# Performance work log

Measured on AMD Instinct MI355X. Metric: run time of the kernel, lower is better.

The kernel has to match this reference:

```python
import jax, jax.numpy as jnp
import numpy as np

ALPHA = 3.0
NNODES, DIM, K = 8192, 64, 32


def setup_inputs() -> dict:
    key = jax.random.key(0)
    ks = jax.random.split(key, 8)
    return {
        "idx": jnp.arange(NNODES, dtype=jnp.int64) if jax.config.jax_enable_x64 else jnp.arange(NNODES, dtype=jnp.int32),
        "emb1": jax.random.normal(ks[0], (NNODES, DIM), dtype=jnp.float32),
        "emb2": jax.random.normal(ks[1], (NNODES, DIM), dtype=jnp.float32),
        "lin1_w": jax.random.normal(ks[2], (DIM, DIM), dtype=jnp.float32) * 0.1,
        "lin1_b": jax.random.normal(ks[3], (DIM,), dtype=jnp.float32) * 0.1,
        "lin2_w": jax.random.normal(ks[4], (DIM, DIM), dtype=jnp.float32) * 0.1,
        "lin2_b": jax.random.normal(ks[5], (DIM,), dtype=jnp.float32) * 0.1,
        "noise": jax.random.uniform(ks[6], (NNODES, NNODES), dtype=jnp.float32),
        "k": K,
    }


def reference(idx, emb1, emb2, lin1_w, lin1_b, lin2_w, lin2_b, noise, k):
    # gather node embeddings, project, tanh(alpha * .)
    nodevec1 = jnp.tanh(ALPHA * (emb1[idx] @ lin1_w.T + lin1_b))  # [N, D]
    nodevec2 = jnp.tanh(ALPHA * (emb2[idx] @ lin2_w.T + lin2_b))  # [N, D]
    # antisymmetric bilinear score
    a = nodevec1 @ nodevec2.T - nodevec2 @ nodevec1.T             # [N, N]
    adj = jax.nn.relu(jnp.tanh(ALPHA * a))                         # [N, N]
    n = adj.shape[0]
    # topk per row with uniform tie-break noise (torch: adj + rand*0.01)
    _, t1 = jax.lax.top_k(adj + noise * 0.01, k)                   # [N, k] int
    rows = jnp.arange(n)[:, None]                                  # [N, 1]
    mask = jnp.zeros((n, n), dtype=adj.dtype).at[rows, t1].set(1.0)
    adj = adj * mask + jnp.eye(n, dtype=adj.dtype)
    return adj
```

## Files before the change

kernel.cpp:

```cpp
#include <hip/hip_runtime.h>

#define NN 8192
#define DD 64
#define CC 128
#define XCLAMP 7.99881172180175781f

__device__ __forceinline__ float guard(float v) {
    asm volatile("" : "+v"(v));
    return v;
}

__device__ __forceinline__ float xla_tanhf(float x) {
    float xc = fminf(fmaxf(x, -XCLAMP), XCLAMP);
    float x2 = xc * xc;
    float p = fmaf(x2, -2.76076847742355e-16f, 2.00018790482477e-13f);
    p = fmaf(x2, p, -8.60467152213735e-11f);
    p = fmaf(x2, p, 5.12229709037114e-08f);
    p = fmaf(x2, p, 1.48572235717979e-05f);
    p = fmaf(x2, p, 6.37261928875436e-04f);
    p = fmaf(x2, p, 4.89352455891786e-03f);
    p = xc * p;
    float q = fmaf(x2, 1.19825839466702e-06f, 1.18534705686654e-04f);
    q = fmaf(x2, q, 2.26843463243900e-03f);
    q = fmaf(x2, q, 4.89352518554385e-03f);
    float r = p / q;
    return (fabsf(x) < 0.0004f) ? x : r;
}

__device__ __forceinline__ float score_of(float a, float nz) {
    float adj = fmaxf(xla_tanhf(3.0f * a), 0.0f);
    float m = guard(0.01f * nz);
    return adj + m;
}

__global__ __launch_bounds__(256) void k1_nodevec(
    const int* __restrict__ idx,
    const float* __restrict__ emb1, const float* __restrict__ emb2,
    const float* __restrict__ w1, const float* __restrict__ b1,
    const float* __restrict__ w2, const float* __restrict__ b2,
    float* __restrict__ Wt)
{
    __shared__ float sw1[64 * 65], sw2[64 * 65];
    __shared__ float sb1[64], sb2[64];
    __shared__ float se1[4][64], se2[4][64];
    int t = threadIdx.x;
    for (int i = t; i < 4096; i += 256) {
        int r = i >> 6, c = i & 63;
        sw1[r * 65 + c] = w1[i];
        sw2[r * 65 + c] = w2[i];
    }
    if (t < 64) { sb1[t] = b1[t]; sb2[t] = b2[t]; }
    int nl = t >> 6, d = t & 63;
    int n = blockIdx.x * 4 + nl;
    bool is64 = (idx[1] == 0);
    int g = (is64 ? idx[2 * n] : idx[n]) & 8191;
    se1[nl][d] = emb1[g * 64 + d];
    se2[nl][d] = emb2[g * 64 + d];
    __syncthreads();
    float z1 = 0.0f, z2 = 0.0f;
#pragma unroll 16
    for (int q = 0; q < 64; ++q) {
        z1 = fmaf(se1[nl][q], sw1[d * 65 + q], z1);
        z2 = fmaf(se2[nl][q], sw2[d * 65 + q], z2);
    }
    z1 = 3.0f * guard(z1 + sb1[d]);
    z2 = 3.0f * guard(z2 + sb2[d]);
    Wt[(size_t)d * NN + n]        = xla_tanhf(z1);
    Wt[(size_t)(64 + d) * NN + n] = xla_tanhf(z2);
}

__global__ __launch_bounds__(256) void k_init(
    float* __restrict__ listVal, int* __restrict__ listIdx)
{
    int i = blockIdx.x * 256 + threadIdx.x;
    listVal[i] = -1.0f;
    listIdx[i] = -1;
}

__global__ __launch_bounds__(512) void k2p_pairscore(
    const float* __restrict__ Wt, const float* __restrict__ noise,
    float* __restrict__ Sc)
{
    __shared__ __align__(16) float smem[17024];
    float* sA1 = smem;
    float* sB1 = smem + 4224;
    float* sA2 = smem + 8448;
    float* sB2 = smem + 12672;
    int bx = blockIdx.x, by = blockIdx.y;
    if (bx < by) return;
    int R = by * 128, C = bx * 128;
    int t = threadIdx.x;
    int ty = t >> 5, tx = t & 31;

    float A1[8][4], A2[8][4];
#pragma unroll
    for (int i = 0; i < 8; ++i)
#pragma unroll
        for (int j = 0; j < 4; ++j) { A1[i][j] = 0.0f; A2[i][j] = 0.0f; }

    for (int kc = 0; kc < 2; ++kc) {
        int k0 = kc * 32;
#pragma unroll
        for (int p = 0; p < 2; ++p) {
            int q = p * 512 + t;
            int kf = q >> 5;
            int rr = (q & 31) * 4;
            float4 v1 = *(const float4*)&Wt[(size_t)(k0 + kf) * NN + R + rr];
            *(float4*)&sA1[kf * 132 + rr] = v1;
            float4 v2 = *(const float4*)&Wt[(size_t)(64 + k0 + kf) * NN + C + rr];
            *(float4*)&sB1[kf * 132 + rr] = v2;
            float4 v3 = *(const float4*)&Wt[(size_t)(64 + k0 + kf) * NN + R + rr];
            *(float4*)&sA2[kf * 132 + rr] = v3;
            float4 v4 = *(const float4*)&Wt[(size_t)(k0 + kf) * NN + C + rr];
            *(float4*)&sB2[kf * 132 + rr] = v4;
        }
        __syncthreads();
#pragma unroll 4
        for (int kk = 0; kk < 32; ++kk) {
            float4 a10 = *(const float4*)&sA1[kk * 132 + ty * 8];
            float4 a11 = *(const float4*)&sA1[kk * 132 + ty * 8 + 4];
            float4 b1v = *(const float4*)&sB1[kk * 132 + tx * 4];
            float4 a20 = *(const float4*)&sA2[kk * 132 + ty * 8];
            float4 a21 = *(const float4*)&sA2[kk * 132 + ty * 8 + 4];
            float4 b2v = *(const float4*)&sB2[kk * 132 + tx * 4];
            float a1[8] = {a10.x, a10.y, a10.z, a10.w, a11.x, a11.y, a11.z, a11.w};
            float b1[4] = {b1v.x, b1v.y, b1v.z, b1v.w};
            float a2[8] = {a20.x, a20.y, a20.z, a20.w, a21.x, a21.y, a21.z, a21.w};
            float b2[4] = {b2v.x, b2v.y, b2v.z, b2v.w};
#pragma unroll
            for (int i = 0; i < 8; ++i)
#pragma unroll
                for (int j = 0; j < 4; ++j) {
                    A1[i][j] = fmaf(a1[i], b1[j], A1[i][j]);
                    A2[i][j] = fmaf(a2[i], b2[j], A2[i][j]);
                }
        }
        __syncthreads();
    }

    float* dT = smem;
#pragma unroll
    for (int i = 0; i < 8; ++i) {
        int I = ty * 8 + i;
        int grow = R + I;
        float4 nz = *(const float4*)&noise[(size_t)grow * NN + C + tx * 4];
        float4 o;
#pragma unroll
        for (int j = 0; j < 4; ++j) {
            float d  = guard(A1[i][j] - A2[i][j]);
            float ta = xla_tanhf(3.0f * fabsf(d));
            float adj1 = (d > 0.0f) ? ta : 0.0f;
            float adj2 = (d < 0.0f) ? ta : 0.0f;
            float m = guard(0.01f * ((const float*)&nz)[j]);
            ((float*)&o)[j] = adj1 + m;
            dT[(tx * 4 + j) * 133 + I] = adj2;
        }
        *(float4*)&Sc[(size_t)grow * NN + C + tx * 4] = o;
    }
    __syncthreads();

    int c4 = tx * 4;
#pragma unroll
    for (int rr = 0; rr < 8; ++rr) {
        int r2 = rr * 16 + ty;
        int grow = C + r2;
        float4 nz = *(const float4*)&noise[(size_t)grow * NN + R + c4];
        float4 o;
        o.x = dT[r2 * 133 + c4 + 0] + guard(0.01f * nz.x);
        o.y = dT[r2 * 133 + c4 + 1] + guard(0.01f * nz.y);
        o.z = dT[r2 * 133 + c4 + 2] + guard(0.01f * nz.z);
        o.w = dT[r2 * 133 + c4 + 3] + guard(0.01f * nz.w);
        *(float4*)&Sc[(size_t)grow * NN + R + c4] = o;
    }
}

__global__ __launch_bounds__(256) void k3_screen(
    const float* __restrict__ Sc,
    float* __restrict__ listVal, int* __restrict__ listIdx)
{
    int lane = threadIdx.x & 63;
    int w    = threadIdx.x >> 6;
    int row  = blockIdx.x * 4 + w;
    const float* Srow = Sc + (size_t)row * NN;

    float Lv = listVal[row * 64 + lane];
    int   Lj = listIdx[row * 64 + lane];

    for (int c0 = 0; c0 < NN; c0 += 256) {
        float s0 = Srow[c0 + lane];
        float s1 = Srow[c0 + 64 + lane];
        float s2 = Srow[c0 + 128 + lane];
        float s3 = Srow[c0 + 192 + lane];
#pragma unroll
        for (int u = 0; u < 4; ++u) {
            float s = (u == 0) ? s0 : (u == 1) ? s1 : (u == 2) ? s2 : s3;
            int jb = c0 + u * 64;
            float tau = __shfl(Lv, 63);
            unsigned long long m = __ballot(s > tau);
            while (m) {
                int b = __ffsll((unsigned long long)m) - 1;
                m &= m - 1;
                float v = __shfl(s, b);
                tau = __shfl(Lv, 63);
                if (v > tau) {
                    float Lu = __shfl_up(Lv, 1);
                    int   Ju = __shfl_up(Lj, 1);
                    bool ge  = (Lv >= v);
                    bool geu = (lane == 0) || (Lu >= v);
                    float nv = ge ? Lv : (geu ? v : Lu);
                    int   nj = ge ? Lj : (geu ? (jb + b) : Ju);
                    Lv = nv; Lj = nj;
                }
            }
        }
    }
    listVal[row * 64 + lane] = Lv;
    listIdx[row * 64 + lane] = Lj;
}

__global__ __launch_bounds__(256) void k4a_fill(float* __restrict__ out)
{
    int i4 = blockIdx.x * 256 + threadIdx.x;
    int f0 = i4 * 4;
    int row = f0 >> 13;
    int colbase = f0 & 8191;
    int drel = row - colbase;
    float4 z = make_float4(0.f, 0.f, 0.f, 0.f);
    if (drel >= 0 && drel < 4) ((float*)&z)[drel] = 1.0f;
    *(float4*)&out[f0] = z;
}

__global__ __launch_bounds__(256) void k4b_scatter(
    const int* __restrict__ listIdx, const float* __restrict__ listVal,
    const float* __restrict__ noise, const int* __restrict__ kptr,
    float* __restrict__ out)
{
    int lane = threadIdx.x & 63;
    int w    = threadIdx.x >> 6;
    int row  = blockIdx.x * 4 + w;
    int kk = kptr[0]; if (kk > 64) kk = 64; if (kk < 1) kk = 1;
    if (lane < kk) {
        int   j = listIdx[row * 64 + lane] & 8191;
        float s = listVal[row * 64 + lane];
        float nz = noise[(size_t)row * NN + j];
        float m = guard(0.01f * nz);
        float adj = s - m;
        if (j == row) adj += 1.0f;
        out[(size_t)row * NN + j] = adj;
    }
}

extern "C" void kernel_launch(void* const* d_in, const int* in_sizes, int n_in,
                              void* d_out, int out_size, void* d_ws, size_t ws_size,
                              hipStream_t stream) {
    (void)in_sizes; (void)n_in; (void)out_size; (void)ws_size;
    const int*   idx   = (const int*)d_in[0];
    const float* emb1  = (const float*)d_in[1];
    const float* emb2  = (const float*)d_in[2];
    const float* w1    = (const float*)d_in[3];
    const float* b1    = (const float*)d_in[4];
    const float* w2    = (const float*)d_in[5];
    const float* b2    = (const float*)d_in[6];
    const float* noise = (const float*)d_in[7];
    const int*   kptr  = (const int*)d_in[8];

    float* out = (float*)d_out;
    float* Sc  = out;

    char*  ws      = (char*)d_ws;
    float* Wt      = (float*)ws;
    float* listVal = (float*)(ws + (size_t)4 * 1024 * 1024);
    int*   listIdx = (int*)  (ws + (size_t)6 * 1024 * 1024);

    k1_nodevec<<<NN / 4, 256, 0, stream>>>(idx, emb1, emb2, w1, b1, w2, b2, Wt);
    k_init<<<NN * 64 / 256, 256, 0, stream>>>(listVal, listIdx);

    dim3 gp(64, 64);
    k2p_pairscore<<<gp, 512, 0, stream>>>(Wt, noise, Sc);

    k3_screen<<<NN / 4, 256, 0, stream>>>(Sc, listVal, listIdx);

    k4a_fill<<<65536, 256, 0, stream>>>(out);
    k4b_scatter<<<NN / 4, 256, 0, stream>>>(listIdx, listVal, noise, kptr, out);
}
```

Baseline: 485.4 us.

## Restructure pair-score GEMM to 256 threads with 8x8 register tiles

The antisymmetric pair-score kernel now uses 256 threads, each computing an 8x8 tile for both products instead of 8x4. It streams a single A/B shared-memory buffer over four K-chunks, using padded B rows to reduce bank conflicts. The transposed lower-triangle output is staged through shared memory in four slices to keep LDS use small. This raises per-thread arithmetic intensity and cuts LDS traffic per FMA, at the cost of higher register pressure (128 accumulators), possibly lower occupancy, and extra barriers.

```diff
diff --git a/kernel.cpp b/kernel.cpp
--- a/kernel.cpp
+++ b/kernel.cpp
@@ -27,12 +27,6 @@
     return (fabsf(x) < 0.0004f) ? x : r;
 }
 
-__device__ __forceinline__ float score_of(float a, float nz) {
-    float adj = fmaxf(xla_tanhf(3.0f * a), 0.0f);
-    float m = guard(0.01f * nz);
-    return adj + m;
-}
-
 __global__ __launch_bounds__(256) void k1_nodevec(
     const int* __restrict__ idx,
     const float* __restrict__ emb1, const float* __restrict__ emb2,
@@ -77,100 +71,116 @@
     listIdx[i] = -1;
 }
 
-__global__ __launch_bounds__(512) void k2p_pairscore(
+__global__ __launch_bounds__(256) void k2p_pairscore(
     const float* __restrict__ Wt, const float* __restrict__ noise,
     float* __restrict__ Sc)
 {
-    __shared__ __align__(16) float smem[17024];
-    float* sA1 = smem;
-    float* sB1 = smem + 4224;
-    float* sA2 = smem + 8448;
-    float* sB2 = smem + 12672;
+    __shared__ __align__(16) float smem[32 * 128 + 32 * 144];
+    float* sA = smem;
+    float* sB = smem + 32 * 128;
     int bx = blockIdx.x, by = blockIdx.y;
     if (bx < by) return;
     int R = by * 128, C = bx * 128;
     int t = threadIdx.x;
-    int ty = t >> 5, tx = t & 31;
-
-    float A1[8][4], A2[8][4];
+    int ty = t >> 4, tx = t & 15;
+
+    float acc1[8][8], acc2[8][8];
 #pragma unroll
     for (int i = 0; i < 8; ++i)
 #pragma unroll
-        for (int j = 0; j < 4; ++j) { A1[i][j] = 0.0f; A2[i][j] = 0.0f; }
-
-    for (int kc = 0; kc < 2; ++kc) {
+        for (int j = 0; j < 8; ++j) { acc1[i][j] = 0.0f; acc2[i][j] = 0.0f; }
+
+    for (int kc = 0; kc < 4; ++kc) {
         int k0 = kc * 32;
-#pragma unroll
-        for (int p = 0; p < 2; ++p) {
-            int q = p * 512 + t;
-            int kf = q >> 5;
-            int rr = (q & 31) * 4;
-            float4 v1 = *(const float4*)&Wt[(size_t)(k0 + kf) * NN + R + rr];
-            *(float4*)&sA1[kf * 132 + rr] = v1;
-            float4 v2 = *(const float4*)&Wt[(size_t)(64 + k0 + kf) * NN + C + rr];
-            *(float4*)&sB1[kf * 132 + rr] = v2;
-            float4 v3 = *(const float4*)&Wt[(size_t)(64 + k0 + kf) * NN + R + rr];
-            *(float4*)&sA2[kf * 132 + rr] = v3;
-            float4 v4 = *(const float4*)&Wt[(size_t)(k0 + kf) * NN + C + rr];
-            *(float4*)&sB2[kf * 132 + rr] = v4;
-        }
-        __syncthreads();
+        int kB = k0 ^ 64;
+#pragma unroll
+        for (int p = 0; p < 4; ++p) {
+            int idx4 = p * 256 + t;
+            int kf = idx4 >> 5;
+            int rr = (idx4 & 31) * 4;
+            float4 av = *(const float4*)&Wt[(size_t)(k0 + kf) * NN + R + rr];
+            *(float4*)&sA[kf * 128 + rr] = av;
+            float4 bv = *(const float4*)&Wt[(size_t)(kB + kf) * NN + C + rr];
+            *(float4*)&sB[kf * 144 + rr + ((rr >> 5) << 2)] = bv;
+        }
+        __syncthreads();
+        bool first = (kc < 2);
+        int boff = tx * 8 + ((tx >> 2) << 2);
 #pragma unroll 4
         for (int kk = 0; kk < 32; ++kk) {
-            float4 a10 = *(const float4*)&sA1[kk * 132 + ty * 8];
-            float4 a11 = *(const float4*)&sA1[kk * 132 + ty * 8 + 4];
-            float4 b1v = *(const float4*)&sB1[kk * 132 + tx * 4];
-            float4 a20 = *(const float4*)&sA2[kk * 132 + ty * 8];
-            float4 a21 = *(const float4*)&sA2[kk * 132 + ty * 8 + 4];
-            float4 b2v = *(const float4*)&sB2[kk * 132 + tx * 4];
-            float a1[8] = {a10.x, a10.y, a10.z, a10.w, a11.x, a11.y, a11.z, a11.w};
-            float b1[4] = {b1v.x, b1v.y, b1v.z, b1v.w};
-            float a2[8] = {a20.x, a20.y, a20.z, a20.w, a21.x, a21.y, a21.z, a21.w};
-            float b2[4] = {b2v.x, b2v.y, b2v.z, b2v.w};
-#pragma unroll
-            for (int i = 0; i < 8; ++i)
-#pragma unroll
-                for (int j = 0; j < 4; ++j) {
-                    A1[i][j] = fmaf(a1[i], b1[j], A1[i][j]);
-                    A2[i][j] = fmaf(a2[i], b2[j], A2[i][j]);
-                }
-        }
-        __syncthreads();
-    }
-
-    float* dT = smem;
+            float4 a0 = *(const float4*)&sA[kk * 128 + ty * 8];
+            float4 a1 = *(const float4*)&sA[kk * 128 + ty * 8 + 4];
+            float4 b0 = *(const float4*)&sB[kk * 144 + boff];
+            float4 b1 = *(const float4*)&sB[kk * 144 + boff + 4];
+            float a[8] = {a0.x, a0.y, a0.z, a0.w, a1.x, a1.y, a1.z, a1.w};
+            float b[8] = {b0.x, b0.y, b0.z, b0.w, b1.x, b1.y, b1.z, b1.w};
+            if (first) {
+#pragma unroll
+                for (int i = 0; i < 8; ++i)
+#pragma unroll
+                    for (int j = 0; j < 8; ++j)
+                        acc1[i][j] = fmaf(a[i], b[j], acc1[i][j]);
+            } else {
+#pragma unroll
+                for (int i = 0; i < 8; ++i)
+#pragma unroll
+                    for (int j = 0; j < 8; ++j)
+                        acc2[i][j] = fmaf(a[i], b[j], acc2[i][j]);
+            }
+        }
+        __syncthreads();
+    }
+
 #pragma unroll
     for (int i = 0; i < 8; ++i) {
-        int I = ty * 8 + i;
-        int grow = R + I;
-        float4 nz = *(const float4*)&noise[(size_t)grow * NN + C + tx * 4];
-        float4 o;
-#pragma unroll
-        for (int j = 0; j < 4; ++j) {
-            float d  = guard(A1[i][j] - A2[i][j]);
+        int grow = R + ty * 8 + i;
+        float4 nz0 = *(const float4*)&noise[(size_t)grow * NN + C + tx * 8];
+        float4 nz1 = *(const float4*)&noise[(size_t)grow * NN + C + tx * 8 + 4];
+        float4 o0, o1;
+#pragma unroll
+        for (int j = 0; j < 8; ++j) {
+            float d  = guard(acc1[i][j] - acc2[i][j]);
             float ta = xla_tanhf(3.0f * fabsf(d));
             float adj1 = (d > 0.0f) ? ta : 0.0f;
             float adj2 = (d < 0.0f) ? ta : 0.0f;
-            float m = guard(0.01f * ((const float*)&nz)[j]);
-            ((float*)&o)[j] = adj1 + m;
-            dT[(tx * 4 + j) * 133 + I] = adj2;
-        }
-        *(float4*)&Sc[(size_t)grow * NN + C + tx * 4] = o;
-    }
-    __syncthreads();
-
-    int c4 = tx * 4;
-#pragma unroll
-    for (int rr = 0; rr < 8; ++rr) {
-        int r2 = rr * 16 + ty;
-        int grow = C + r2;
-        float4 nz = *(const float4*)&noise[(size_t)grow * NN + R + c4];
-        float4 o;
-        o.x = dT[r2 * 133 + c4 + 0] + guard(0.01f * nz.x);
-        o.y = dT[r2 * 133 + c4 + 1] + guard(0.01f * nz.y);
-        o.z = dT[r2 * 133 + c4 + 2] + guard(0.01f * nz.z);
-        o.w = dT[r2 * 133 + c4 + 3] + guard(0.01f * nz.w);
-        *(float4*)&Sc[(size_t)grow * NN + R + c4] = o;
+            float nzj = (j < 4) ? ((const float*)&nz0)[j] : ((const float*)&nz1)[j - 4];
+            float m = guard(0.01f * nzj);
+            float sc = adj1 + m;
+            if (j < 4) ((float*)&o0)[j] = sc; else ((float*)&o1)[j - 4] = sc;
+            acc2[i][j] = adj2;
+        }
+        *(float4*)&Sc[(size_t)grow * NN + C + tx * 8]     = o0;
+        *(float4*)&Sc[(size_t)grow * NN + C + tx * 8 + 4] = o1;
+    }
+
+    float* dT = smem;
+#pragma unroll
+    for (int s = 0; s < 4; ++s) {
+        __syncthreads();
+        if ((ty >> 2) == s) {
+            int base = (ty & 3) * 8;
+#pragma unroll
+            for (int i = 0; i < 8; ++i)
+#pragma unroll
+                for (int j = 0; j < 8; ++j)
+                    dT[(tx * 8 + j) * 33 + base + i] = acc2[i][j];
+        }
+        __syncthreads();
+#pragma unroll
+        for (int p = 0; p < 4; ++p) {
+            int idx = p * 256 + t;
+            int J  = idx >> 3;
+            int c4 = (idx & 7) * 4;
+            int grow = C + J;
+            int gcol = R + 32 * s + c4;
+            float4 nz = *(const float4*)&noise[(size_t)grow * NN + gcol];
+            float4 o;
+            o.x = dT[J * 33 + c4 + 0] + guard(0.01f * nz.x);
+            o.y = dT[J * 33 + c4 + 1] + guard(0.01f * nz.y);
+            o.z = dT[J * 33 + c4 + 2] + guard(0.01f * nz.z);
+            o.w = dT[J * 33 + c4 + 3] + guard(0.01f * nz.w);
+            *(float4*)&Sc[(size_t)grow * NN + gcol] = o;
+        }
     }
 }
 
@@ -276,7 +286,7 @@
     k_init<<<NN * 64 / 256, 256, 0, stream>>>(listVal, listIdx);
 
     dim3 gp(64, 64);
-    k2p_pairscore<<<gp, 512, 0, stream>>>(Wt, noise, Sc);
+    k2p_pairscore<<<gp, 256, 0, stream>>>(Wt, noise, Sc);
 
     k3_screen<<<NN / 4, 256, 0, stream>>>(Sc, listVal, listIdx);
 
```

Result: slower. 621.2 us (+28.0%).
